# Kernel tuning notes

Hardware: AMD Instinct MI355X
Metric: run time of the kernel (lower is better)

Reference implementation:

```python
import jax, jax.numpy as jnp
import numpy as np

T, N, E, D_IN, D_OUT = 8, 50000, 800000, 64, 64


def setup_inputs() -> dict:
    key = jax.random.key(0)
    k = jax.random.split(key, 7)
    x = jax.random.normal(k[0], (T, N, D_IN), dtype=jnp.float32)
    edge_index = jax.random.randint(k[1], (2, E), 0, N, dtype=jnp.int32)
    edge_time = jax.random.uniform(k[2], (E,), dtype=jnp.float32)
    node_time = jnp.sort(jax.random.uniform(k[3], (T,), dtype=jnp.float32))
    edge_weight = jax.random.uniform(k[4], (E,), dtype=jnp.float32)
    W = jax.random.normal(k[5], (D_IN, D_OUT), dtype=jnp.float32) / jnp.sqrt(jnp.float32(D_IN))
    b = jnp.zeros((D_OUT,), dtype=jnp.float32)
    return {"x": x, "edge_index": edge_index, "edge_time": edge_time,
            "node_time": node_time, "edge_weight": edge_weight, "W": W, "b": b}


def reference(x, edge_index, edge_time, node_time, edge_weight, W, b):
    # Faithful translation of DGN.forward: per-timestep temporal GNN conv.
    # DGNConv (assumed canonical form): edges with edge_time <= node_time[i]
    # are active; messages x[src]*edge_weight are sum-scattered to dst, then a
    # Linear(in, out) is applied. lax.scan replaces the Python time loop.
    src, dst = edge_index[0], edge_index[1]

    def step(_, xt_t):
        xt, t = xt_t  # xt: [N, D_IN], t: scalar
        w = jnp.where(edge_time <= t, edge_weight, jnp.float32(0.0))  # [E]
        msg = xt[src] * w[:, None]                                    # [E, D_IN]
        agg = jax.ops.segment_sum(msg, dst, num_segments=N)           # [N, D_IN]
        return None, agg @ W + b                                      # [N, D_OUT]

    _, out = jax.lax.scan(step, None, (x, node_time))
    return out  # [T, N, D_OUT]
```

## Files before the change

kernel.cpp:

```cpp
#include <hip/hip_runtime.h>
#include <cstdint>
#include <cstddef>

#define TSTEPS 8
#define D 64

static __device__ __forceinline__ unsigned short f2bf(float f) {
    unsigned int u = __float_as_uint(f);
    unsigned int r = (u + 0x7FFFu + ((u >> 16) & 1u)) >> 16;
    return (unsigned short)r;
}
static __device__ __forceinline__ float bf2f(unsigned short h) {
    return __uint_as_float(((unsigned int)h) << 16);
}

__global__ void hist_kernel(const int* __restrict__ dst, int E, int* __restrict__ cnt) {
    int e = blockIdx.x * blockDim.x + threadIdx.x;
    if (e < E) atomicAdd(&cnt[dst[e]], 1);
}

__global__ __launch_bounds__(256) void reduce_kernel(const int* __restrict__ cnt,
                                                     int* __restrict__ sums, int n) {
    __shared__ int red[256];
    int tid = threadIdx.x;
    int base = blockIdx.x * 1024 + tid * 4;
    int tot = 0;
#pragma unroll
    for (int j = 0; j < 4; j++) { int i = base + j; tot += (i < n) ? cnt[i] : 0; }
    red[tid] = tot;
    __syncthreads();
    for (int s = 128; s > 0; s >>= 1) {
        if (tid < s) red[tid] += red[tid + s];
        __syncthreads();
    }
    if (tid == 0) sums[blockIdx.x] = red[0];
}

__global__ __launch_bounds__(256) void scanwrite_kernel(const int* __restrict__ cnt,
                                                        const int* __restrict__ sums,
                                                        int* __restrict__ rowptr,
                                                        int* __restrict__ fill,
                                                        int n, int E) {
    __shared__ int buf[256];
    int tid = threadIdx.x;
    int base = blockIdx.x * 1024 + tid * 4;
    int v[4];
    int tot = 0;
#pragma unroll
    for (int j = 0; j < 4; j++) { int i = base + j; v[j] = (i < n) ? cnt[i] : 0; tot += v[j]; }

    buf[tid] = tot;
    __syncthreads();
    for (int off = 1; off < 256; off <<= 1) {
        int t = (tid >= off) ? buf[tid - off] : 0;
        __syncthreads();
        buf[tid] += t;
        __syncthreads();
    }
    int exclThread = buf[tid] - tot;

    int bp = 0;
    for (int j = 0; j < blockIdx.x; j++) bp += sums[j];

    int running = bp + exclThread;
#pragma unroll
    for (int j = 0; j < 4; j++) {
        int i = base + j;
        if (i < n) { rowptr[i] = running; fill[i] = running; running += v[j]; }
    }
    if (blockIdx.x == 0 && tid == 0) rowptr[n] = E;
}

__global__ __launch_bounds__(256) void bucket_kernel(
    const int* __restrict__ src, const int* __restrict__ dst,
    const float* __restrict__ etime, const float* __restrict__ ew,
    const float* __restrict__ ntime, int E,
    int* __restrict__ fill, uint2* __restrict__ meta)
{
    int e = blockIdx.x * blockDim.x + threadIdx.x;
    if (e >= E) return;
    float et = etime[e];
    int t0 = 0;
#pragma unroll
    for (int t = 0; t < TSTEPS; t++) t0 += (ntime[t] < et) ? 1 : 0;
    unsigned int lo = ((unsigned int)src[e] << 4) | (unsigned int)t0;
    uint2 m;
    m.x = lo;
    m.y = __float_as_uint(ew[e]);
    int p = atomicAdd(&fill[dst[e]], 1);
    meta[p] = m;
}

__global__ __launch_bounds__(256) void cvt_kernel(const float* __restrict__ x,
                                                  unsigned short* __restrict__ xb,
                                                  long n4) {
    long i = (long)blockIdx.x * blockDim.x + threadIdx.x;
    if (i >= n4) return;
    float4 v = ((const float4*)x)[i];
    ushort4 u;
    u.x = f2bf(v.x); u.y = f2bf(v.y); u.z = f2bf(v.z); u.w = f2bf(v.w);
    ((ushort4*)xb)[i] = u;
}

template<bool USE_BF16>
__global__ __launch_bounds__(256) void fused_gather_kernel(
    const float* __restrict__ xf, const unsigned short* __restrict__ xb,
    const uint2* __restrict__ meta, const int* __restrict__ rowptr,
    const float* __restrict__ W, const float* __restrict__ b,
    float* __restrict__ out, int N)
{
    __shared__ float Wlds[64 * 64];
    __shared__ float aggS[4][TSTEPS][64];

    int tid = threadIdx.x;
#pragma unroll
    for (int i = 0; i < 16; i++) Wlds[tid + i * 256] = W[tid + i * 256];
    __syncthreads();

    int wslot = tid >> 6;
    int lane  = tid & 63;
    int g = lane >> 4;
    int q = lane & 15;
    int n = blockIdx.x * 4 + wslot;

    const size_t plane  = (size_t)N * D;
    const size_t plane4 = plane >> 2;

    float4 acc[TSTEPS];
#pragma unroll
    for (int t = 0; t < TSTEPS; t++) acc[t] = make_float4(0.f, 0.f, 0.f, 0.f);

    if (n < N) {
        int p0 = rowptr[n], p1 = rowptr[n + 1];
        for (int p = p0; p < p1; p += 4) {
            int idx = p + g;
            int s = 0, t0 = TSTEPS;
            float w = 0.f;
            if (idx < p1) {
                uint2 m = meta[idx];
                s  = (int)(m.x >> 4);
                t0 = (int)(m.x & 15u);
                w  = __uint_as_float(m.y);
            }
            if (USE_BF16) {
                const unsigned short* xp = xb + (size_t)s * D + q * 4;
#pragma unroll
                for (int t = 0; t < TSTEPS; t++) {
                    if (t >= t0) {
                        ushort4 u = *reinterpret_cast<const ushort4*>(xp + (size_t)t * plane);
                        acc[t].x = fmaf(bf2f(u.x), w, acc[t].x);
                        acc[t].y = fmaf(bf2f(u.y), w, acc[t].y);
                        acc[t].z = fmaf(bf2f(u.z), w, acc[t].z);
                        acc[t].w = fmaf(bf2f(u.w), w, acc[t].w);
                    }
                }
            } else {
                const float4* xp = reinterpret_cast<const float4*>(xf + (size_t)s * D) + q;
#pragma unroll
                for (int t = 0; t < TSTEPS; t++) {
                    if (t >= t0) {
                        float4 v = xp[(size_t)t * plane4];
                        acc[t].x = fmaf(v.x, w, acc[t].x);
                        acc[t].y = fmaf(v.y, w, acc[t].y);
                        acc[t].z = fmaf(v.z, w, acc[t].z);
                        acc[t].w = fmaf(v.w, w, acc[t].w);
                    }
                }
            }
        }
    }

#pragma unroll
    for (int t = 0; t < TSTEPS; t++) {
        acc[t].x += __shfl_xor(acc[t].x, 16); acc[t].y += __shfl_xor(acc[t].y, 16);
        acc[t].z += __shfl_xor(acc[t].z, 16); acc[t].w += __shfl_xor(acc[t].w, 16);
        acc[t].x += __shfl_xor(acc[t].x, 32); acc[t].y += __shfl_xor(acc[t].y, 32);
        acc[t].z += __shfl_xor(acc[t].z, 32); acc[t].w += __shfl_xor(acc[t].w, 32);
    }

    if (lane < 16) {
#pragma unroll
        for (int t = 0; t < TSTEPS; t++)
            *reinterpret_cast<float4*>(&aggS[wslot][t][lane * 4]) = acc[t];
    }
    __syncthreads();

    float o[TSTEPS];
    float bias = b[lane];
#pragma unroll
    for (int t = 0; t < TSTEPS; t++) o[t] = bias;

    for (int kc = 0; kc < 16; kc++) {
        float w0 = Wlds[(4 * kc + 0) * 64 + lane];
        float w1 = Wlds[(4 * kc + 1) * 64 + lane];
        float w2 = Wlds[(4 * kc + 2) * 64 + lane];
        float w3 = Wlds[(4 * kc + 3) * 64 + lane];
#pragma unroll
        for (int t = 0; t < TSTEPS; t++) {
            float4 a = *reinterpret_cast<const float4*>(&aggS[wslot][t][4 * kc]);
            o[t] = fmaf(a.x, w0, fmaf(a.y, w1, fmaf(a.z, w2, fmaf(a.w, w3, o[t]))));
        }
    }

    if (n < N) {
        size_t ob = (size_t)n * D + lane;
#pragma unroll
        for (int t = 0; t < TSTEPS; t++) out[(size_t)t * plane + ob] = o[t];
    }
}

extern "C" void kernel_launch(void* const* d_in, const int* in_sizes, int n_in,
                              void* d_out, int out_size, void* d_ws, size_t ws_size,
                              hipStream_t stream)
{
    const float* x     = (const float*)d_in[0];
    const int*   eidx  = (const int*)d_in[1];
    const float* etime = (const float*)d_in[2];
    const float* ntime = (const float*)d_in[3];
    const float* ew    = (const float*)d_in[4];
    const float* W     = (const float*)d_in[5];
    const float* b     = (const float*)d_in[6];
    float* out = (float*)d_out;

    const int T = in_sizes[3];
    const int E = in_sizes[1] / 2;
    const int N = in_sizes[0] / (T * D);

    const int* src = eidx;
    const int* dst = eidx + E;

    char* base = (char*)d_ws;
    uint2* meta  = (uint2*)base;
    int* cnt     = (int*)(base + 8ll * E);
    int* rowptr  = cnt + N;
    int* fill    = rowptr + N + 1;
    int* sums    = fill + N;
    size_t off = 8ll * E + 4ll * (3ll * N + 1 + 64);
    off = (off + 15) & ~(size_t)15;
    unsigned short* xb = (unsigned short*)(base + off);
    size_t need = off + 2ll * T * N * D;
    bool useBf16 = (ws_size >= need);

    hipMemsetAsync(cnt, 0, (size_t)N * sizeof(int), stream);

    hist_kernel<<<(E + 255) / 256, 256, 0, stream>>>(dst, E, cnt);

    int nb = (N + 1023) / 1024;
    reduce_kernel<<<nb, 256, 0, stream>>>(cnt, sums, N);
    scanwrite_kernel<<<nb, 256, 0, stream>>>(cnt, sums, rowptr, fill, N, E);

    bucket_kernel<<<(E + 255) / 256, 256, 0, stream>>>(src, dst, etime, ew, ntime,
                                                       E, fill, meta);

    if (useBf16) {
        long n4 = (long)T * N * D / 4;
        cvt_kernel<<<(int)((n4 + 255) / 256), 256, 0, stream>>>(x, xb, n4);
        fused_gather_kernel<true><<<(N + 3) / 4, 256, 0, stream>>>(
            x, xb, meta, rowptr, W, b, out, N);
    } else {
        fused_gather_kernel<false><<<(N + 3) / 4, 256, 0, stream>>>(
            x, xb, meta, rowptr, W, b, out, N);
    }
}
```

Baseline: 497.1 us.

## Bucket edges by destination and activation timestep to remove per-timestep predication

Builds the CSR over (dst, first active timestep) keys, so each node has 8 sub-rows instead of 1. The gather kernel then loops per timestep over the cumulative prefix of active edges, so no per-edge predication is needed inside the timestep loop. Edges never active in any step are dropped. The histogram pass now records each edge's key and rank, so the bucket pass writes directly to its final slot without a second atomic. In exchange, each edge's metadata is reread once per timestep it is active, and the counter and scan arrays become eight times larger.

```diff
diff --git a/kernel.cpp b/kernel.cpp
--- a/kernel.cpp
+++ b/kernel.cpp
@@ -7,16 +7,32 @@
 
 static __device__ __forceinline__ unsigned short f2bf(float f) {
     unsigned int u = __float_as_uint(f);
-    unsigned int r = (u + 0x7FFFu + ((u >> 16) & 1u)) >> 16;
-    return (unsigned short)r;
+    return (unsigned short)((u + 0x7FFFu + ((u >> 16) & 1u)) >> 16);
 }
 static __device__ __forceinline__ float bf2f(unsigned short h) {
     return __uint_as_float(((unsigned int)h) << 16);
 }
 
-__global__ void hist_kernel(const int* __restrict__ dst, int E, int* __restrict__ cnt) {
-    int e = blockIdx.x * blockDim.x + threadIdx.x;
-    if (e < E) atomicAdd(&cnt[dst[e]], 1);
+__global__ __launch_bounds__(256) void hist_kernel(
+    const int* __restrict__ dst, const float* __restrict__ etime,
+    const float* __restrict__ ntime, int E,
+    int* __restrict__ cnt, unsigned int* __restrict__ keyA,
+    unsigned int* __restrict__ rankA)
+{
+    int e = blockIdx.x * 256 + threadIdx.x;
+    if (e >= E) return;
+    float et = etime[e];
+    int t0 = 0;
+#pragma unroll
+    for (int t = 0; t < TSTEPS; t++) t0 += (ntime[t] < et) ? 1 : 0;
+    if (t0 < TSTEPS) {
+        unsigned int key = ((unsigned int)dst[e] << 3) | (unsigned int)t0;
+        unsigned int r = (unsigned int)atomicAdd(&cnt[key], 1);
+        keyA[e] = key;
+        rankA[e] = r;
+    } else {
+        keyA[e] = 0xFFFFFFFFu;
+    }
 }
 
 __global__ __launch_bounds__(256) void reduce_kernel(const int* __restrict__ cnt,
@@ -38,9 +54,7 @@
 
 __global__ __launch_bounds__(256) void scanwrite_kernel(const int* __restrict__ cnt,
                                                         const int* __restrict__ sums,
-                                                        int* __restrict__ rowptr,
-                                                        int* __restrict__ fill,
-                                                        int n, int E) {
+                                                        int* __restrict__ rowptr, int n) {
     __shared__ int buf[256];
     int tid = threadIdx.x;
     int base = blockIdx.x * 1024 + tid * 4;
@@ -66,28 +80,24 @@
 #pragma unroll
     for (int j = 0; j < 4; j++) {
         int i = base + j;
-        if (i < n) { rowptr[i] = running; fill[i] = running; running += v[j]; }
-    }
-    if (blockIdx.x == 0 && tid == 0) rowptr[n] = E;
+        if (i < n) { rowptr[i] = running; running += v[j]; }
+    }
+    if (blockIdx.x == (int)gridDim.x - 1 && tid == 255) rowptr[n] = running;
 }
 
 __global__ __launch_bounds__(256) void bucket_kernel(
-    const int* __restrict__ src, const int* __restrict__ dst,
-    const float* __restrict__ etime, const float* __restrict__ ew,
-    const float* __restrict__ ntime, int E,
-    int* __restrict__ fill, uint2* __restrict__ meta)
-{
-    int e = blockIdx.x * blockDim.x + threadIdx.x;
+    const int* __restrict__ src, const float* __restrict__ ew, int E,
+    const unsigned int* __restrict__ keyA, const unsigned int* __restrict__ rankA,
+    const int* __restrict__ rowptr, uint2* __restrict__ meta)
+{
+    int e = blockIdx.x * 256 + threadIdx.x;
     if (e >= E) return;
-    float et = etime[e];
-    int t0 = 0;
-#pragma unroll
-    for (int t = 0; t < TSTEPS; t++) t0 += (ntime[t] < et) ? 1 : 0;
-    unsigned int lo = ((unsigned int)src[e] << 4) | (unsigned int)t0;
+    unsigned int key = keyA[e];
+    if (key == 0xFFFFFFFFu) return;
+    int p = rowptr[key] + (int)rankA[e];
     uint2 m;
-    m.x = lo;
+    m.x = (unsigned int)src[e];
     m.y = __float_as_uint(ew[e]);
-    int p = atomicAdd(&fill[dst[e]], 1);
     meta[p] = m;
 }
 
@@ -123,43 +133,58 @@
     int q = lane & 15;
     int n = blockIdx.x * 4 + wslot;
 
-    const size_t plane  = (size_t)N * D;
-    const size_t plane4 = plane >> 2;
+    const size_t plane = (size_t)N * D;
 
     float4 acc[TSTEPS];
 #pragma unroll
     for (int t = 0; t < TSTEPS; t++) acc[t] = make_float4(0.f, 0.f, 0.f, 0.f);
 
     if (n < N) {
-        int p0 = rowptr[n], p1 = rowptr[n + 1];
-        for (int p = p0; p < p1; p += 4) {
-            int idx = p + g;
-            int s = 0, t0 = TSTEPS;
-            float w = 0.f;
-            if (idx < p1) {
-                uint2 m = meta[idx];
-                s  = (int)(m.x >> 4);
-                t0 = (int)(m.x & 15u);
-                w  = __uint_as_float(m.y);
-            }
+        int rbase = n * 8;
+        int base = rowptr[rbase];
+#pragma unroll
+        for (int t = 0; t < TSTEPS; t++) {
+            int end = rowptr[rbase + t + 1];
             if (USE_BF16) {
-                const unsigned short* xp = xb + (size_t)s * D + q * 4;
-#pragma unroll
-                for (int t = 0; t < TSTEPS; t++) {
-                    if (t >= t0) {
-                        ushort4 u = *reinterpret_cast<const ushort4*>(xp + (size_t)t * plane);
+                const unsigned short* xp = xb + (size_t)t * plane + q * 4;
+                for (int p = base; p < end; p += 8) {
+                    int i0 = p + g, i1 = p + g + 4;
+                    if (i0 < end) {
+                        uint2 m = meta[i0];
+                        float w = __uint_as_float(m.y);
+                        ushort4 u = *reinterpret_cast<const ushort4*>(xp + ((size_t)m.x << 6));
                         acc[t].x = fmaf(bf2f(u.x), w, acc[t].x);
                         acc[t].y = fmaf(bf2f(u.y), w, acc[t].y);
                         acc[t].z = fmaf(bf2f(u.z), w, acc[t].z);
                         acc[t].w = fmaf(bf2f(u.w), w, acc[t].w);
                     }
+                    if (i1 < end) {
+                        uint2 m = meta[i1];
+                        float w = __uint_as_float(m.y);
+                        ushort4 u = *reinterpret_cast<const ushort4*>(xp + ((size_t)m.x << 6));
+                        acc[t].x = fmaf(bf2f(u.x), w, acc[t].x);
+                        acc[t].y = fmaf(bf2f(u.y), w, acc[t].y);
+                        acc[t].z = fmaf(bf2f(u.z), w, acc[t].z);
+                        acc[t].w = fmaf(bf2f(u.w), w, acc[t].w);
+                    }
                 }
             } else {
-                const float4* xp = reinterpret_cast<const float4*>(xf + (size_t)s * D) + q;
-#pragma unroll
-                for (int t = 0; t < TSTEPS; t++) {
-                    if (t >= t0) {
-                        float4 v = xp[(size_t)t * plane4];
+                const float4* xp = reinterpret_cast<const float4*>(xf + (size_t)t * plane) + q;
+                for (int p = base; p < end; p += 8) {
+                    int i0 = p + g, i1 = p + g + 4;
+                    if (i0 < end) {
+                        uint2 m = meta[i0];
+                        float w = __uint_as_float(m.y);
+                        float4 v = xp[(size_t)m.x << 4];
+                        acc[t].x = fmaf(v.x, w, acc[t].x);
+                        acc[t].y = fmaf(v.y, w, acc[t].y);
+                        acc[t].z = fmaf(v.z, w, acc[t].z);
+                        acc[t].w = fmaf(v.w, w, acc[t].w);
+                    }
+                    if (i1 < end) {
+                        uint2 m = meta[i1];
+                        float w = __uint_as_float(m.y);
+                        float4 v = xp[(size_t)m.x << 4];
                         acc[t].x = fmaf(v.x, w, acc[t].x);
                         acc[t].y = fmaf(v.y, w, acc[t].y);
                         acc[t].z = fmaf(v.z, w, acc[t].z);
@@ -225,32 +250,37 @@
     const int T = in_sizes[3];
     const int E = in_sizes[1] / 2;
     const int N = in_sizes[0] / (T * D);
+    const int N8 = N * 8;
 
     const int* src = eidx;
     const int* dst = eidx + E;
 
+    int nb = (N8 + 1023) / 1024;
+
     char* base = (char*)d_ws;
-    uint2* meta  = (uint2*)base;
-    int* cnt     = (int*)(base + 8ll * E);
-    int* rowptr  = cnt + N;
-    int* fill    = rowptr + N + 1;
-    int* sums    = fill + N;
-    size_t off = 8ll * E + 4ll * (3ll * N + 1 + 64);
-    off = (off + 15) & ~(size_t)15;
-    unsigned short* xb = (unsigned short*)(base + off);
-    size_t need = off + 2ll * T * N * D;
-    bool useBf16 = (ws_size >= need);
-
-    hipMemsetAsync(cnt, 0, (size_t)N * sizeof(int), stream);
-
-    hist_kernel<<<(E + 255) / 256, 256, 0, stream>>>(dst, E, cnt);
-
-    int nb = (N + 1023) / 1024;
-    reduce_kernel<<<nb, 256, 0, stream>>>(cnt, sums, N);
-    scanwrite_kernel<<<nb, 256, 0, stream>>>(cnt, sums, rowptr, fill, N, E);
-
-    bucket_kernel<<<(E + 255) / 256, 256, 0, stream>>>(src, dst, etime, ew, ntime,
-                                                       E, fill, meta);
+    uint2* meta   = (uint2*)base;
+    int*   cnt    = (int*)(base + 8ll * E);
+    int*   rowptr = cnt + N8;
+    int*   sums   = rowptr + N8 + 1;
+    size_t offK = 8ll * E + 4ll * (2ll * N8 + 1 + nb);
+    offK = (offK + 15) & ~(size_t)15;
+    unsigned int* keyA  = (unsigned int*)(base + offK);
+    unsigned int* rankA = keyA + E;
+    unsigned short* xb  = (unsigned short*)(base + offK);
+
+    size_t xbBytes = 2ll * T * N * D;
+    size_t krBytes = 8ll * E;
+    size_t needB = offK + (xbBytes > krBytes ? xbBytes : krBytes);
+    bool useBf16 = (ws_size >= needB);
+
+    hipMemsetAsync(cnt, 0, (size_t)N8 * sizeof(int), stream);
+
+    hist_kernel<<<(E + 255) / 256, 256, 0, stream>>>(dst, etime, ntime, E,
+                                                     cnt, keyA, rankA);
+    reduce_kernel<<<nb, 256, 0, stream>>>(cnt, sums, N8);
+    scanwrite_kernel<<<nb, 256, 0, stream>>>(cnt, sums, rowptr, N8);
+    bucket_kernel<<<(E + 255) / 256, 256, 0, stream>>>(src, ew, E, keyA, rankA,
+                                                       rowptr, meta);
 
     if (useBf16) {
         long n4 = (long)T * N * D / 4;
```

Result: slower. 515.7 us (+3.7%).
